# Kernel tuning notes

Measured on AMD Instinct MI355X. Metric: run time of the kernel, lower is better.

The kernel has to match this reference:

```python
import jax, jax.numpy as jnp
import numpy as np

K = 25        # moving_avg_window
PAD = (K - 1) // 2
EPS = 1e-8


def _decompose(x):
    # x: [B, S, C]
    B, S, C = x.shape
    # --- trend: AvgPool1d(kernel=K, stride=1, padding=PAD), count_include_pad=True
    # zero-pad then windowed sum, always divide by K (matches torch default).
    sums = jax.lax.reduce_window(
        x, jnp.float32(0.0).astype(x.dtype), jax.lax.add,
        window_dimensions=(1, K, 1), window_strides=(1, 1, 1),
        padding=((0, 0), (PAD, PAD), (0, 0)))
    trend = sums / K  # [B, S, C]

    # --- initial seasonal: FFT along time, zero out first half of bins
    # (including DC), take real part of inverse FFT.
    half = S // 2
    freq_mask = (jnp.arange(S) >= half)[None, :, None]  # [1, S, 1]
    dft = jnp.fft.fft(x, axis=1)
    seasonal0 = jnp.fft.ifft(dft * freq_mask, axis=1).real.astype(x.dtype)

    # --- degrees of trend/seasonality per (batch, channel)
    # Reference uses the robust fallback residual = x - trend - seasonal0
    # (the STL path in the original is a per-series scipy call; its fallback
    # defines the same math).
    resid = x - trend - seasonal0
    var = lambda v: jnp.var(v, axis=1, ddof=1)  # torch.var is unbiased -> ddof=1; [B, C]
    var_res = var(resid)
    d_t = jnp.clip(1.0 - var_res / (var(trend + resid) + EPS), 0.0, 1.0)
    d_s = jnp.clip(1.0 - var_res / (var(seasonal0 + resid) + EPS), 0.0, 1.0)

    # --- final seasonal: multiplicative if strong trend/seasonality, else additive
    cond = ((d_t > 0.5) | (d_s > 0.5))[:, None, :]  # [B, 1, C]
    seasonal = jnp.where(cond, x / (trend + EPS), x - trend)
    return trend, seasonal


def setup_inputs() -> dict:
    key = jax.random.key(0)
    x = jax.random.normal(key, (32, 4096, 128), dtype=jnp.float32)
    return {"x": x}


def reference(x):
    return _decompose(x)
```

## Files before the change

kernel.cpp:

```cpp
#include <hip/hip_runtime.h>

#define SS 4096
#define CC 128
#define BB 32
#define KW 25
#define PADW 12
#define CH 64
#define SROWS (CH + KW - 1)
#define CPB 8
#define HC 64
#define HCP 32
#define NSERIES (BB * CC)
#define STAGE_F4 (SROWS * HC / 4)

typedef float f4v __attribute__((ext_vector_type(4)));
typedef float f2v __attribute__((ext_vector_type(2)));

__global__ __launch_bounds__(512)
void kb_pass(const float* __restrict__ x, float* __restrict__ trend,
             float* __restrict__ seasonal, float* __restrict__ stats) {
    __shared__ f4v stage[2][STAGE_F4];

    const int blk = blockIdx.x;
    const int b = blk >> 4;
    const int q = (blk >> 1) & 7;
    const int h = blk & 1;
    const int tid = threadIdx.x;
    const int cp = tid & 31;
    const int rg = tid >> 5;
    const float* __restrict__ xbh = x + (size_t)b * SS * CC + h * HC;
    f2v* __restrict__ tb2 = (f2v*)(trend + (size_t)b * SS * CC);
    f2v* __restrict__ sv2 = (f2v*)(seasonal + (size_t)b * SS * CC);
    const int co = h * HCP + 0;

    {
        const int sbase = q * (CPB * CH) - PADW;
        #pragma unroll
        for (int t = 0; t < 3; ++t) {
            const int idx = t * 512 + tid;
            if (idx < STAGE_F4) {
                const int srow = sbase + (idx >> 4);
                const int crow = srow < 0 ? 0 : (srow >= SS ? SS - 1 : srow);
                f4v v = *(const f4v*)(xbh + (size_t)crow * CC + ((idx & 15) << 2));
                if (srow < 0 || srow >= SS) v = (f4v){0.f, 0.f, 0.f, 0.f};
                stage[0][idx] = v;
            }
        }
    }

    f4v vals[2];
    auto issue = [&](int c) {
        const int sbase = q * (CPB * CH) + c * CH - PADW;
        #pragma unroll
        for (int t = 0; t < 2; ++t) {
            const int nidx = t * 512 + tid;
            const int srow = sbase + 24 + (nidx >> 4);
            const int crow = srow >= SS ? SS - 1 : srow;
            vals[t] = *(const f4v*)(xbh + (size_t)crow * CC + ((nidx & 15) << 2));
        }
    };
    auto commit = [&](int c, int buf) {
        const f2v* src = (const f2v*)stage[buf ^ 1];
        f2v* dst = (f2v*)stage[buf];
        #pragma unroll
        for (int t = 0; t < 2; ++t) {
            const int hidx = t * 512 + tid;
            if (hidx < 24 * HCP) dst[hidx] = src[CH * HCP + hidx];
        }
        const int sbase = q * (CPB * CH) + c * CH - PADW;
        #pragma unroll
        for (int t = 0; t < 2; ++t) {
            const int nidx = t * 512 + tid;
            const int srow = sbase + 24 + (nidx >> 4);
            f4v w = vals[t];
            if (srow >= SS) w = (f4v){0.f, 0.f, 0.f, 0.f};
            stage[buf][384 + nidx] = w;
        }
    };

    f2v Sx_e = {0,0}, Sx_o = {0,0}, Sx2 = {0,0};
    f2v St_e = {0,0}, St_o = {0,0}, St2 = {0,0}, Sxt = {0,0};

    for (int c = 0; c < CPB; ++c) {
        __syncthreads();
        const int cur = c & 1;
        if (c + 1 < CPB) issue(c + 1);

        const int S0 = q * (CPB * CH) + c * CH;
        const int r0 = rg * 4;
        const f2v* stg = (const f2v*)stage[cur];

        f2v win[KW];
        #pragma unroll
        for (int j = 0; j < KW; ++j) win[j] = stg[(r0 + j) * HCP + cp];

        #pragma unroll
        for (int i = 0; i < 4; ++i) {
            float ax = win[0].x, ay = win[0].y;
            #pragma unroll
            for (int j = 1; j < KW; ++j) { ax += win[j].x; ay += win[j].y; }
            f2v tf;
            tf.x = ax / 25.0f;
            tf.y = ay / 25.0f;
            const int row = (S0 + r0 + i) * 64 + co + cp;
            __builtin_nontemporal_store(tf, &tb2[row]);

            const f2v xv = win[PADW];
            f2v so;
            so.x = xv.x / (tf.x + 1e-8f);
            so.y = xv.y / (tf.y + 1e-8f);
            __builtin_nontemporal_store(so, &sv2[row]);

            if (i & 1) { Sx_o.x += xv.x; Sx_o.y += xv.y; St_o.x += tf.x; St_o.y += tf.y; }
            else       { Sx_e.x += xv.x; Sx_e.y += xv.y; St_e.x += tf.x; St_e.y += tf.y; }
            Sx2.x += xv.x * xv.x;  Sx2.y += xv.y * xv.y;
            St2.x += tf.x * tf.x;  St2.y += tf.y * tf.y;
            Sxt.x += xv.x * tf.x;  Sxt.y += xv.y * tf.y;

            #pragma unroll
            for (int j = 0; j < KW - 1; ++j) win[j] = win[j + 1];
            if (i < 3) win[KW - 1] = stg[(r0 + i + KW) * HCP + cp];
        }

        if (c + 1 < CPB) commit(c + 1, cur ^ 1);
    }

    __syncthreads();
    f2v* sr = (f2v*)stage;
    if (rg > 0) {
        f2v* me = sr + (size_t)(rg - 1) * 7 * HCP + cp;
        me[0*HCP] = Sx_e; me[1*HCP] = Sx_o; me[2*HCP] = Sx2;
        me[3*HCP] = St_e; me[4*HCP] = St_o; me[5*HCP] = St2;
        me[6*HCP] = Sxt;
    }
    __syncthreads();
    if (rg == 0) {
        #pragma unroll
        for (int g = 0; g < 15; ++g) {
            const f2v* gp = sr + (size_t)g * 7 * HCP + cp;
            Sx_e.x += gp[0*HCP].x; Sx_e.y += gp[0*HCP].y;
            Sx_o.x += gp[1*HCP].x; Sx_o.y += gp[1*HCP].y;
            Sx2.x  += gp[2*HCP].x; Sx2.y  += gp[2*HCP].y;
            St_e.x += gp[3*HCP].x; St_e.y += gp[3*HCP].y;
            St_o.x += gp[4*HCP].x; St_o.y += gp[4*HCP].y;
            St2.x  += gp[5*HCP].x; St2.y  += gp[5*HCP].y;
            Sxt.x  += gp[6*HCP].x; Sxt.y  += gp[6*HCP].y;
        }
        const int series = b * CC + h * HC + 2 * cp;
        float* sp = stats + (size_t)q * NSERIES + series;
        const size_t jstride = (size_t)CPB * NSERIES;
        *(f2v*)(sp + 0 * jstride) = Sx_e;
        *(f2v*)(sp + 1 * jstride) = Sx_o;
        *(f2v*)(sp + 2 * jstride) = Sx2;
        *(f2v*)(sp + 3 * jstride) = St_e;
        *(f2v*)(sp + 4 * jstride) = St_o;
        *(f2v*)(sp + 5 * jstride) = St2;
        *(f2v*)(sp + 6 * jstride) = Sxt;
    }
}

__global__ __launch_bounds__(256)
void k2_finalize_fix(const float* __restrict__ stats, const float* __restrict__ x,
                     const float* __restrict__ trend, float* __restrict__ seasonal) {
    const int j = threadIdx.x >> 5;
    const int sl = threadIdx.x & 31;
    const int series0 = blockIdx.x * 32;
    const size_t jstride = (size_t)CPB * NSERIES;

    __shared__ float red[32][8];
    __shared__ int nf;
    __shared__ int flist[32];
    if (threadIdx.x == 0) nf = 0;
    if (j < 7) {
        const float* p = stats + j * jstride + series0 + sl;
        float a = 0.f;
        #pragma unroll
        for (int k = 0; k < CPB; ++k) a += p[(size_t)k * NSERIES];
        red[sl][j] = a;
    }
    __syncthreads();
    if (threadIdx.x < 32) {
        const int me = threadIdx.x;
        const float Sx_e = red[me][0], Sx_o = red[me][1], Sx2 = red[me][2];
        const float St_e = red[me][3], St_o = red[me][4], St2 = red[me][5];
        const float Sxt = red[me][6];

        const float Sf = (float)SS;
        const float halfS = 0.5f * Sf;
        const float c_e = Sx_o / Sf;
        const float c_o = Sx_e / Sf;
        const float sum_c = halfS * (c_e + c_o);
        const float sumsq_c = halfS * (c_e * c_e + c_o * c_o);

        const float Sw_e = 0.5f * Sx_e - St_e;
        const float Sw_o = 0.5f * Sx_o - St_o;
        const float Sw2 = 0.25f * Sx2 - Sxt + St2;

        const float s1 = (Sw_e + Sw_o) + sum_c;
        const float q1 = Sw2 + 2.f * (c_e * Sw_e + c_o * Sw_o) + sumsq_c;
        const float var1 = (q1 - s1 * s1 / Sf) / (Sf - 1.f);
        const float s2 = 0.5f * (Sx_e + Sx_o) + sum_c;
        const float q2 = 0.25f * Sx2 + (c_e * Sx_e + c_o * Sx_o) + sumsq_c;
        const float var2 = (q2 - s2 * s2 / Sf) / (Sf - 1.f);
        const float Sa = (Sx_e + Sx_o) - (St_e + St_o);
        const float Sa2 = Sx2 - 2.f * Sxt + St2;
        const float var3 = (Sa2 - Sa * Sa / Sf) / (Sf - 1.f);

        const float d_t = 1.f - var1 / (var2 + 1e-8f);
        const float d_s = 1.f - var1 / (var3 + 1e-8f);
        if (!(d_t > 0.5f || d_s > 0.5f)) {
            const int i = atomicAdd(&nf, 1);
            flist[i] = series0 + me;
        }
    }
    __syncthreads();
    for (int fi = 0; fi < nf; ++fi) {
        const int sr = flist[fi];
        const int b = sr >> 7, ch = sr & 127;
        const float* xs = x + (size_t)b * SS * CC + ch;
        const float* ts = trend + (size_t)b * SS * CC + ch;
        float* so = seasonal + (size_t)b * SS * CC + ch;
        for (int s = threadIdx.x; s < SS; s += 256)
            so[(size_t)s * CC] = xs[(size_t)s * CC] - ts[(size_t)s * CC];
    }
}

extern "C" void kernel_launch(void* const* d_in, const int* in_sizes, int n_in,
                              void* d_out, int out_size, void* d_ws, size_t ws_size,
                              hipStream_t stream) {
    const float* x = (const float*)d_in[0];
    float* out = (float*)d_out;
    float* trend = out;
    float* seasonal = out + (size_t)BB * SS * CC;

    float* stats = (float*)d_ws;

    kb_pass<<<dim3(BB * 16), dim3(512), 0, stream>>>(x, trend, seasonal, stats);
    k2_finalize_fix<<<dim3(NSERIES / 32), dim3(256), 0, stream>>>(stats, x, trend, seasonal);
}
```

Before: 39.85 us.

## Fuse finalize/fix pass into main kernel via last-block ticket per batch

Removes the second kernel launch by having the last of each batch's 16 blocks, chosen through an atomic ticket counter, reduce the partial stats and rewrite additive-mode channels. This saves a kernel launch and its dependency gap but adds a memset launch, threadfences, and serialized tail work on one block per batch. Extra shared memory for the finalize buffers may lower occupancy.

```diff
diff --git a/kernel.cpp b/kernel.cpp
--- a/kernel.cpp
+++ b/kernel.cpp
@@ -18,8 +18,12 @@
 
 __global__ __launch_bounds__(512)
 void kb_pass(const float* __restrict__ x, float* __restrict__ trend,
-             float* __restrict__ seasonal, float* __restrict__ stats) {
+             float* __restrict__ seasonal, float* __restrict__ stats,
+             int* __restrict__ cnt) {
     __shared__ f4v stage[2][STAGE_F4];
+    __shared__ float fin[7][128];
+    __shared__ int ticket_s, nf;
+    __shared__ int flist[128];
 
     const int blk = blockIdx.x;
     const int b = blk >> 4;
@@ -31,7 +35,7 @@
     const float* __restrict__ xbh = x + (size_t)b * SS * CC + h * HC;
     f2v* __restrict__ tb2 = (f2v*)(trend + (size_t)b * SS * CC);
     f2v* __restrict__ sv2 = (f2v*)(seasonal + (size_t)b * SS * CC);
-    const int co = h * HCP + 0;
+    const int co = h * HCP;
 
     {
         const int sbase = q * (CPB * CH) - PADW;
@@ -157,70 +161,68 @@
         *(f2v*)(sp + 5 * jstride) = St2;
         *(f2v*)(sp + 6 * jstride) = Sxt;
     }
-}
-
-__global__ __launch_bounds__(256)
-void k2_finalize_fix(const float* __restrict__ stats, const float* __restrict__ x,
-                     const float* __restrict__ trend, float* __restrict__ seasonal) {
-    const int j = threadIdx.x >> 5;
-    const int sl = threadIdx.x & 31;
-    const int series0 = blockIdx.x * 32;
-    const size_t jstride = (size_t)CPB * NSERIES;
-
-    __shared__ float red[32][8];
-    __shared__ int nf;
-    __shared__ int flist[32];
-    if (threadIdx.x == 0) nf = 0;
-    if (j < 7) {
-        const float* p = stats + j * jstride + series0 + sl;
-        float a = 0.f;
-        #pragma unroll
-        for (int k = 0; k < CPB; ++k) a += p[(size_t)k * NSERIES];
-        red[sl][j] = a;
-    }
-    __syncthreads();
-    if (threadIdx.x < 32) {
-        const int me = threadIdx.x;
-        const float Sx_e = red[me][0], Sx_o = red[me][1], Sx2 = red[me][2];
-        const float St_e = red[me][3], St_o = red[me][4], St2 = red[me][5];
-        const float Sxt = red[me][6];
+
+    __syncthreads();
+    if (tid == 0) {
+        __threadfence();
+        ticket_s = atomicAdd(&cnt[b], 1);
+    }
+    __syncthreads();
+    if (ticket_s != 15) return;
+    __threadfence();
+
+    if (tid < 448) {
+        const int j = tid >> 6, c2 = tid & 63;
+        const float* p = stats + (size_t)j * CPB * NSERIES + b * CC + 2 * c2;
+        f2v a = {0.f, 0.f};
+        #pragma unroll
+        for (int k = 0; k < CPB; ++k) {
+            const f2v v = *(const f2v*)(p + (size_t)k * NSERIES);
+            a.x += v.x; a.y += v.y;
+        }
+        fin[j][2 * c2] = a.x; fin[j][2 * c2 + 1] = a.y;
+    }
+    if (tid == 0) nf = 0;
+    __syncthreads();
+    if (tid < 128) {
+        const int ch = tid;
+        const float Sx_eF = fin[0][ch], Sx_oF = fin[1][ch], Sx2F = fin[2][ch];
+        const float St_eF = fin[3][ch], St_oF = fin[4][ch], St2F = fin[5][ch];
+        const float SxtF = fin[6][ch];
 
         const float Sf = (float)SS;
         const float halfS = 0.5f * Sf;
-        const float c_e = Sx_o / Sf;
-        const float c_o = Sx_e / Sf;
+        const float c_e = Sx_oF / Sf;
+        const float c_o = Sx_eF / Sf;
         const float sum_c = halfS * (c_e + c_o);
         const float sumsq_c = halfS * (c_e * c_e + c_o * c_o);
 
-        const float Sw_e = 0.5f * Sx_e - St_e;
-        const float Sw_o = 0.5f * Sx_o - St_o;
-        const float Sw2 = 0.25f * Sx2 - Sxt + St2;
+        const float Sw_e = 0.5f * Sx_eF - St_eF;
+        const float Sw_o = 0.5f * Sx_oF - St_oF;
+        const float Sw2 = 0.25f * Sx2F - SxtF + St2F;
 
         const float s1 = (Sw_e + Sw_o) + sum_c;
         const float q1 = Sw2 + 2.f * (c_e * Sw_e + c_o * Sw_o) + sumsq_c;
         const float var1 = (q1 - s1 * s1 / Sf) / (Sf - 1.f);
-        const float s2 = 0.5f * (Sx_e + Sx_o) + sum_c;
-        const float q2 = 0.25f * Sx2 + (c_e * Sx_e + c_o * Sx_o) + sumsq_c;
+        const float s2 = 0.5f * (Sx_eF + Sx_oF) + sum_c;
+        const float q2 = 0.25f * Sx2F + (c_e * Sx_eF + c_o * Sx_oF) + sumsq_c;
         const float var2 = (q2 - s2 * s2 / Sf) / (Sf - 1.f);
-        const float Sa = (Sx_e + Sx_o) - (St_e + St_o);
-        const float Sa2 = Sx2 - 2.f * Sxt + St2;
+        const float Sa = (Sx_eF + Sx_oF) - (St_eF + St_oF);
+        const float Sa2 = Sx2F - 2.f * SxtF + St2F;
         const float var3 = (Sa2 - Sa * Sa / Sf) / (Sf - 1.f);
 
         const float d_t = 1.f - var1 / (var2 + 1e-8f);
         const float d_s = 1.f - var1 / (var3 + 1e-8f);
-        if (!(d_t > 0.5f || d_s > 0.5f)) {
-            const int i = atomicAdd(&nf, 1);
-            flist[i] = series0 + me;
-        }
+        if (!(d_t > 0.5f || d_s > 0.5f))
+            flist[atomicAdd(&nf, 1)] = ch;
     }
     __syncthreads();
     for (int fi = 0; fi < nf; ++fi) {
-        const int sr = flist[fi];
-        const int b = sr >> 7, ch = sr & 127;
+        const int ch = flist[fi];
         const float* xs = x + (size_t)b * SS * CC + ch;
         const float* ts = trend + (size_t)b * SS * CC + ch;
         float* so = seasonal + (size_t)b * SS * CC + ch;
-        for (int s = threadIdx.x; s < SS; s += 256)
+        for (int s = tid; s < SS; s += 512)
             so[(size_t)s * CC] = xs[(size_t)s * CC] - ts[(size_t)s * CC];
     }
 }
@@ -234,7 +236,9 @@
     float* seasonal = out + (size_t)BB * SS * CC;
 
     float* stats = (float*)d_ws;
-
-    kb_pass<<<dim3(BB * 16), dim3(512), 0, stream>>>(x, trend, seasonal, stats);
-    k2_finalize_fix<<<dim3(NSERIES / 32), dim3(256), 0, stream>>>(stats, x, trend, seasonal);
+    int* cnt = (int*)(stats + 7 * CPB * NSERIES);
+
+    hipMemsetAsync(cnt, 0, BB * sizeof(int), stream);
+    kb_pass<<<dim3(BB * 16), dim3(512), 0, stream>>>(x, trend, seasonal,
+                                                     stats, cnt);
 }
```

After: 89.05 us. 2.23x slower.
